# Kernel optimization log

Hardware: AMD Instinct MI355X
Metric: run time of the kernel (lower is better)

The kernel has to match this reference:

```python
import jax, jax.numpy as jnp
import numpy as np

N, DIN, DOUT = 8192, 256, 128
NEG_SLOPE = 0.01         # F.leaky_relu default
MASK_VAL = -9.0e15       # from the torch source


def setup_inputs() -> dict:
    key = jax.random.key(0)
    kx, kadj, kW, kbW, ka1, ka2, kba = jax.random.split(key, 7)
    x = jax.random.normal(kx, (N, DIN), dtype=jnp.float32)
    adj = jax.random.randint(kadj, (N, N), 0, 2, dtype=jnp.int32)
    # Linear W: input_dim -> output_dim
    W = jax.random.normal(kW, (DIN, DOUT), dtype=jnp.float32) * (1.0 / np.sqrt(DIN))
    bW = jax.random.normal(kbW, (DOUT,), dtype=jnp.float32) * 0.01
    # Linear a: 2*output_dim -> 1, split into the h_i part (a1) and h_j part (a2)
    a1 = jax.random.normal(ka1, (DOUT,), dtype=jnp.float32) * (1.0 / np.sqrt(2 * DOUT))
    a2 = jax.random.normal(ka2, (DOUT,), dtype=jnp.float32) * (1.0 / np.sqrt(2 * DOUT))
    ba = jax.random.normal(kba, (), dtype=jnp.float32) * 0.01
    return {"x": x, "adj": adj, "W": W, "bW": bW, "a1": a1, "a2": a2, "ba": ba}


def reference(x, adj, W, bW, a1, a2, ba):
    # h = W x + b  -> [N, DOUT]
    h = x @ W + bW
    # e[i,j] = leaky_relu(a . [h_i, h_j] + ba) = leaky_relu(a1.h_i + a2.h_j + ba)
    s_src = h @ a1            # [N]
    s_dst = h @ a2            # [N]
    e = s_src[:, None] + s_dst[None, :] + ba   # [N, N]
    e = jnp.where(e > 0, e, NEG_SLOPE * e)
    # mask non-edges, row softmax over neighbors j
    e = jnp.where(adj > 0, e, MASK_VAL)
    alpha = jax.nn.softmax(e, axis=1)          # [N, N]
    # dropout is identity in eval mode (dropout_rate=0)
    return alpha @ h                            # [N, DOUT]
```

## Files before the change

### kernel.cpp

```cpp
#include <hip/hip_runtime.h>
#include <hip/hip_bf16.h>


#define NN 8192
#define DIN 256
#define DOUT 128
#define LOG2E 1.4426950408889634f

typedef __attribute__((ext_vector_type(8))) short short8;
typedef __attribute__((ext_vector_type(4))) float floatx4;

__global__ void prep_wt(const float* __restrict__ W, __hip_bfloat16* __restrict__ WT) {
    int e = blockIdx.x * blockDim.x + threadIdx.x;
    if (e < DIN * DOUT) {
        int k = e >> 7;
        int d = e & 127;
        WT[d * DIN + k] = __float2bfloat16(W[e]);
    }
}

__global__ __launch_bounds__(256, 4) void gat_h(
    const float* __restrict__ x, const __hip_bfloat16* __restrict__ WT,
    const float* __restrict__ bW, const float* __restrict__ a1, const float* __restrict__ a2,
    __hip_bfloat16* __restrict__ hbB, float* __restrict__ s_src, float* __restrict__ s_dst) {
    int tid = threadIdx.x;
    int w = tid >> 6, lane = tid & 63;
    int lm = lane & 15, lq = lane >> 4;
    int i0 = blockIdx.x * 32;
    int r0 = (w >> 1) * 16;
    int c0 = (w & 1) * 64;

    __shared__ float s1s[32], s2s[32];
    if (tid < 32) { s1s[tid] = 0.f; s2s[tid] = 0.f; }
    __syncthreads();

    floatx4 acc[4] = {};
#pragma unroll
    for (int kk = 0; kk < DIN; kk += 32) {
        const float4* xp = (const float4*)&x[(size_t)(i0 + r0 + lm) * DIN + kk + lq * 8];
        float4 xa = xp[0], xb = xp[1];
        union { short8 v; __hip_bfloat16 h[8]; } af;
        af.h[0] = __float2bfloat16(xa.x); af.h[1] = __float2bfloat16(xa.y);
        af.h[2] = __float2bfloat16(xa.z); af.h[3] = __float2bfloat16(xa.w);
        af.h[4] = __float2bfloat16(xb.x); af.h[5] = __float2bfloat16(xb.y);
        af.h[6] = __float2bfloat16(xb.z); af.h[7] = __float2bfloat16(xb.w);
#pragma unroll
        for (int t = 0; t < 4; t++) {
            int d = c0 + 16 * t + lm;
            short8 bf = *(const short8*)&WT[(size_t)d * DIN + kk + lq * 8];
            acc[t] = __builtin_amdgcn_mfma_f32_16x16x32_bf16(af.v, bf, acc[t], 0, 0, 0);
        }
    }
    float s1[4] = {0.f, 0.f, 0.f, 0.f}, s2[4] = {0.f, 0.f, 0.f, 0.f};
#pragma unroll
    for (int t = 0; t < 4; t++) {
        int d = c0 + 16 * t + lm;
        int f = (c0 >> 4) + t;
        float A1 = a1[d], A2 = a2[d], B = bW[d];
#pragma unroll
        for (int r = 0; r < 4; r++) {
            int k = r0 + lq * 4 + r;
            float h = acc[t][r] + B;
            hbB[(size_t)blockIdx.x * 4096 + f * 512 + (k >> 3) * 128 + lm * 8 + (k & 7)] =
                __float2bfloat16(h);
            s1[r] += h * A1;
            s2[r] += h * A2;
        }
    }
#pragma unroll
    for (int r = 0; r < 4; r++) {
        for (int m = 1; m < 16; m <<= 1) {
            s1[r] += __shfl_xor(s1[r], m, 64);
            s2[r] += __shfl_xor(s2[r], m, 64);
        }
    }
    if (lm == 0) {
#pragma unroll
        for (int r = 0; r < 4; r++) {
            int row = r0 + lq * 4 + r;
            atomicAdd(&s1s[row], s1[r]);
            atomicAdd(&s2s[row], s2[r]);
        }
    }
    __syncthreads();
    if (tid < 32) {
        s_src[i0 + tid] = s1s[tid] * LOG2E;
        s_dst[i0 + tid] = s2s[tid] * LOG2E;
    }
}

template <int NJT>
__global__ void build_mask(const int* __restrict__ adj, unsigned char* __restrict__ mask) {
    size_t gid = (size_t)blockIdx.x * blockDim.x + threadIdx.x;
    const int4* a = (const int4*)(adj + gid * 8);
    int4 v0 = a[0], v1 = a[1];
    unsigned int b = 0;
    b |= (v0.x != 0) ? 1u : 0u;
    b |= (v0.y != 0) ? 2u : 0u;
    b |= (v0.z != 0) ? 4u : 0u;
    b |= (v0.w != 0) ? 8u : 0u;
    b |= (v1.x != 0) ? 16u : 0u;
    b |= (v1.y != 0) ? 32u : 0u;
    b |= (v1.z != 0) ? 64u : 0u;
    b |= (v1.w != 0) ? 128u : 0u;
    unsigned int g = (unsigned int)gid & (NJT * 4 - 1);
    size_t pos = (gid & ~(size_t)(NJT * 4 - 1)) | ((g & 3) * NJT + (g >> 2));
    mask[pos] = (unsigned char)b;
}

template <int NJT>
__global__ __launch_bounds__(256, 4) void gat_attn(
    const unsigned char* __restrict__ mask, const float* __restrict__ s_src,
    const float* __restrict__ s_dst, const float* __restrict__ ba_p,
    const __hip_bfloat16* __restrict__ hbB,
    float* __restrict__ num, float* __restrict__ lpart) {
    int tid = threadIdx.x;
    int w = tid >> 6, lane = tid & 63;
    int lm = lane & 15, lq = lane >> 4;
    int b = blockIdx.x;
    int ib = b & 127;
    int jh = b >> 7;
    int i0 = ib * 64 + w * 16;
    int jb0 = jh * (NJT * 32);

    const unsigned char* mrow = mask + (size_t)(i0 + lm) * (NN / 8) + jh * (NJT * 4) + lq * NJT;
    union { uint4 v[NJT / 16]; unsigned int u[NJT / 4]; } mr;
#pragma unroll
    for (int q = 0; q < NJT / 16; q++) mr.v[q] = ((const uint4*)mrow)[q];

    float ssi = s_src[i0 + lm] + ba_p[0] * LOG2E;
    const float* sd = s_dst + jb0 + lq * 8;
    const __hip_bfloat16* hb = hbB + ((size_t)(jh * NJT) * 8) * 512 + lane * 8;

    floatx4 acc[8] = {};
    floatx4 accd = {};
    const short8 ones = { 0x3F80, 0x3F80, 0x3F80, 0x3F80, 0x3F80, 0x3F80, 0x3F80, 0x3F80 };

#pragma unroll
    for (int t = 0; t < NJT; t++) {
        unsigned int cm = (mr.u[t >> 2] >> ((t & 3) * 8)) & 0xFFu;
        float4 cd0 = *(const float4*)(sd + t * 32);
        float4 cd1 = *(const float4*)(sd + t * 32 + 4);
        float p[8];
        {
            float e;
            e = ssi + cd0.x; e = fmaxf(e, 0.01f * e); p[0] = (cm & 1u)   ? __builtin_amdgcn_exp2f(e) : 0.f;
            e = ssi + cd0.y; e = fmaxf(e, 0.01f * e); p[1] = (cm & 2u)   ? __builtin_amdgcn_exp2f(e) : 0.f;
            e = ssi + cd0.z; e = fmaxf(e, 0.01f * e); p[2] = (cm & 4u)   ? __builtin_amdgcn_exp2f(e) : 0.f;
            e = ssi + cd0.w; e = fmaxf(e, 0.01f * e); p[3] = (cm & 8u)   ? __builtin_amdgcn_exp2f(e) : 0.f;
            e = ssi + cd1.x; e = fmaxf(e, 0.01f * e); p[4] = (cm & 16u)  ? __builtin_amdgcn_exp2f(e) : 0.f;
            e = ssi + cd1.y; e = fmaxf(e, 0.01f * e); p[5] = (cm & 32u)  ? __builtin_amdgcn_exp2f(e) : 0.f;
            e = ssi + cd1.z; e = fmaxf(e, 0.01f * e); p[6] = (cm & 64u)  ? __builtin_amdgcn_exp2f(e) : 0.f;
            e = ssi + cd1.w; e = fmaxf(e, 0.01f * e); p[7] = (cm & 128u) ? __builtin_amdgcn_exp2f(e) : 0.f;
        }
        union { short8 v; __hip_bfloat162 q[4]; } af;
        af.q[0] = __float22bfloat162_rn(make_float2(p[0], p[1]));
        af.q[1] = __float22bfloat162_rn(make_float2(p[2], p[3]));
        af.q[2] = __float22bfloat162_rn(make_float2(p[4], p[5]));
        af.q[3] = __float22bfloat162_rn(make_float2(p[6], p[7]));

        const __hip_bfloat16* hbt = hb + (size_t)t * 8 * 512;
#pragma unroll
        for (int f = 0; f < 8; f++) {
            short8 bf = *(const short8*)(hbt + f * 512);
            acc[f] = __builtin_amdgcn_mfma_f32_16x16x32_bf16(af.v, bf, acc[f], 0, 0, 0);
        }
        accd = __builtin_amdgcn_mfma_f32_16x16x32_bf16(af.v, ones, accd, 0, 0, 0);
    }

    float* nb = num + ((size_t)jh * NN + i0) * DOUT;
#pragma unroll
    for (int f = 0; f < 8; f++)
#pragma unroll
        for (int r = 0; r < 4; r++)
            nb[(size_t)(lq * 4 + r) * DOUT + f * 16 + lm] = acc[f][r];
    if (lm == 0) {
#pragma unroll
        for (int r = 0; r < 4; r++)
            lpart[(size_t)jh * NN + i0 + lq * 4 + r] = accd[r];
    }
}

__global__ void gat_combine(const float* __restrict__ num, const float* __restrict__ lpart,
                            float* __restrict__ out, int jsplit) {
    int gid = blockIdx.x * blockDim.x + threadIdx.x;
    int idx = gid * 4;
    int i = idx >> 7;
    float den = 0.f;
    for (int s = 0; s < jsplit; s++) den += lpart[(size_t)s * NN + i];
    float inv = 1.0f / den;
    float4 o = make_float4(0.f, 0.f, 0.f, 0.f);
    for (int s = 0; s < jsplit; s++) {
        float4 n = *(const float4*)&num[(size_t)s * NN * DOUT + idx];
        o.x += n.x; o.y += n.y; o.z += n.z; o.w += n.w;
    }
    o.x *= inv; o.y *= inv; o.z *= inv; o.w *= inv;
    *(float4*)&out[idx] = o;
}

extern "C" void kernel_launch(void* const* d_in, const int* in_sizes, int n_in,
                              void* d_out, int out_size, void* d_ws, size_t ws_size,
                              hipStream_t stream) {
    const float* x  = (const float*)d_in[0];
    const int* adj  = (const int*)d_in[1];
    const float* W  = (const float*)d_in[2];
    const float* bW = (const float*)d_in[3];
    const float* a1 = (const float*)d_in[4];
    const float* a2 = (const float*)d_in[5];
    const float* ba = (const float*)d_in[6];
    float* out = (float*)d_out;

    char* ws = (char*)d_ws;
    __hip_bfloat16* hbB  = (__hip_bfloat16*)ws;
    __hip_bfloat16* WT   = (__hip_bfloat16*)(ws + 2097152);
    float* s_src         = (float*)(ws + 2162688);
    float* s_dst         = (float*)(ws + 2195456);
    float* lpart         = (float*)(ws + 2228224);
    unsigned char* mask  = (unsigned char*)(ws + 2490368);
    float* num           = (float*)(ws + 10878976);

    int jsplit = (ws_size >= 10878976 + (size_t)8 * NN * DOUT * 4) ? 8 : 4;

    prep_wt<<<128, 256, 0, stream>>>(W, WT);
    gat_h<<<256, 256, 0, stream>>>(x, WT, bW, a1, a2, hbB, s_src, s_dst);
    if (jsplit == 8) {
        build_mask<32><<<32768, 256, 0, stream>>>(adj, mask);
        gat_attn<32><<<1024, 256, 0, stream>>>(mask, s_src, s_dst, ba, hbB, num, lpart);
    } else {
        build_mask<64><<<32768, 256, 0, stream>>>(adj, mask);
        gat_attn<64><<<512, 256, 0, stream>>>(mask, s_src, s_dst, ba, hbB, num, lpart);
    }
    gat_combine<<<1024, 256, 0, stream>>>(num, lpart, out, jsplit);
}
```

Measured before the change: 459.1 us.

## Compute two 16-row tiles per wave to reuse h fragments across MFMAs

Each wave now handles 32 query rows (two 16-row MFMA tiles) instead of 16. Every loaded bf16 h fragment feeds two MFMAs, which halves h load traffic per unit of work. The j dimension is split into 16 chunks instead of 8 so the grid stays at 1024 blocks, and launch bounds drop to 3 waves per SIMD to leave room for the doubled accumulator registers. The costs are larger partial-sum buffers for the combine kernel, more register pressure and lower occupancy.

```diff
diff --git a/kernel.cpp b/kernel.cpp
--- a/kernel.cpp
+++ b/kernel.cpp
@@ -108,8 +108,29 @@
     mask[pos] = (unsigned char)b;
 }
 
+__device__ inline short8 make_pfrag(unsigned int cm, float ssi, float4 cd0, float4 cd1,
+                                    floatx4* accd, const short8 ones) {
+    float p[8];
+    float e;
+    e = ssi + cd0.x; e = fmaxf(e, 0.01f * e); p[0] = (cm & 1u)   ? __builtin_amdgcn_exp2f(e) : 0.f;
+    e = ssi + cd0.y; e = fmaxf(e, 0.01f * e); p[1] = (cm & 2u)   ? __builtin_amdgcn_exp2f(e) : 0.f;
+    e = ssi + cd0.z; e = fmaxf(e, 0.01f * e); p[2] = (cm & 4u)   ? __builtin_amdgcn_exp2f(e) : 0.f;
+    e = ssi + cd0.w; e = fmaxf(e, 0.01f * e); p[3] = (cm & 8u)   ? __builtin_amdgcn_exp2f(e) : 0.f;
+    e = ssi + cd1.x; e = fmaxf(e, 0.01f * e); p[4] = (cm & 16u)  ? __builtin_amdgcn_exp2f(e) : 0.f;
+    e = ssi + cd1.y; e = fmaxf(e, 0.01f * e); p[5] = (cm & 32u)  ? __builtin_amdgcn_exp2f(e) : 0.f;
+    e = ssi + cd1.z; e = fmaxf(e, 0.01f * e); p[6] = (cm & 64u)  ? __builtin_amdgcn_exp2f(e) : 0.f;
+    e = ssi + cd1.w; e = fmaxf(e, 0.01f * e); p[7] = (cm & 128u) ? __builtin_amdgcn_exp2f(e) : 0.f;
+    union { short8 v; __hip_bfloat162 q[4]; } af;
+    af.q[0] = __float22bfloat162_rn(make_float2(p[0], p[1]));
+    af.q[1] = __float22bfloat162_rn(make_float2(p[2], p[3]));
+    af.q[2] = __float22bfloat162_rn(make_float2(p[4], p[5]));
+    af.q[3] = __float22bfloat162_rn(make_float2(p[6], p[7]));
+    *accd = __builtin_amdgcn_mfma_f32_16x16x32_bf16(af.v, ones, *accd, 0, 0, 0);
+    return af.v;
+}
+
 template <int NJT>
-__global__ __launch_bounds__(256, 4) void gat_attn(
+__global__ __launch_bounds__(256, 3) void gat_attn(
     const unsigned char* __restrict__ mask, const float* __restrict__ s_src,
     const float* __restrict__ s_dst, const float* __restrict__ ba_p,
     const __hip_bfloat16* __restrict__ hbB,
@@ -118,66 +139,63 @@
     int w = tid >> 6, lane = tid & 63;
     int lm = lane & 15, lq = lane >> 4;
     int b = blockIdx.x;
-    int ib = b & 127;
-    int jh = b >> 7;
-    int i0 = ib * 64 + w * 16;
+    int ib = b & 63;
+    int jh = b >> 6;
+    int i0 = ib * 128 + w * 32;
     int jb0 = jh * (NJT * 32);
 
-    const unsigned char* mrow = mask + (size_t)(i0 + lm) * (NN / 8) + jh * (NJT * 4) + lq * NJT;
-    union { uint4 v[NJT / 16]; unsigned int u[NJT / 4]; } mr;
-#pragma unroll
-    for (int q = 0; q < NJT / 16; q++) mr.v[q] = ((const uint4*)mrow)[q];
-
-    float ssi = s_src[i0 + lm] + ba_p[0] * LOG2E;
+    const unsigned char* mrow0 = mask + (size_t)(i0 + lm) * (NN / 8) + jh * (NJT * 4) + lq * NJT;
+    const unsigned char* mrow1 = mrow0 + (size_t)16 * (NN / 8);
+    union Mr { uint4 v[NJT / 16]; unsigned int u[NJT / 4]; };
+    Mr mr0, mr1;
+#pragma unroll
+    for (int q = 0; q < NJT / 16; q++) {
+        mr0.v[q] = ((const uint4*)mrow0)[q];
+        mr1.v[q] = ((const uint4*)mrow1)[q];
+    }
+
+    float ba = ba_p[0] * LOG2E;
+    float ssi0 = s_src[i0 + lm] + ba;
+    float ssi1 = s_src[i0 + 16 + lm] + ba;
     const float* sd = s_dst + jb0 + lq * 8;
     const __hip_bfloat16* hb = hbB + ((size_t)(jh * NJT) * 8) * 512 + lane * 8;
 
-    floatx4 acc[8] = {};
-    floatx4 accd = {};
+    floatx4 acc0[8] = {}, acc1[8] = {};
+    floatx4 accd0 = {}, accd1 = {};
     const short8 ones = { 0x3F80, 0x3F80, 0x3F80, 0x3F80, 0x3F80, 0x3F80, 0x3F80, 0x3F80 };
 
 #pragma unroll
     for (int t = 0; t < NJT; t++) {
-        unsigned int cm = (mr.u[t >> 2] >> ((t & 3) * 8)) & 0xFFu;
+        unsigned int cm0 = (mr0.u[t >> 2] >> ((t & 3) * 8)) & 0xFFu;
+        unsigned int cm1 = (mr1.u[t >> 2] >> ((t & 3) * 8)) & 0xFFu;
         float4 cd0 = *(const float4*)(sd + t * 32);
         float4 cd1 = *(const float4*)(sd + t * 32 + 4);
-        float p[8];
-        {
-            float e;
-            e = ssi + cd0.x; e = fmaxf(e, 0.01f * e); p[0] = (cm & 1u)   ? __builtin_amdgcn_exp2f(e) : 0.f;
-            e = ssi + cd0.y; e = fmaxf(e, 0.01f * e); p[1] = (cm & 2u)   ? __builtin_amdgcn_exp2f(e) : 0.f;
-            e = ssi + cd0.z; e = fmaxf(e, 0.01f * e); p[2] = (cm & 4u)   ? __builtin_amdgcn_exp2f(e) : 0.f;
-            e = ssi + cd0.w; e = fmaxf(e, 0.01f * e); p[3] = (cm & 8u)   ? __builtin_amdgcn_exp2f(e) : 0.f;
-            e = ssi + cd1.x; e = fmaxf(e, 0.01f * e); p[4] = (cm & 16u)  ? __builtin_amdgcn_exp2f(e) : 0.f;
-            e = ssi + cd1.y; e = fmaxf(e, 0.01f * e); p[5] = (cm & 32u)  ? __builtin_amdgcn_exp2f(e) : 0.f;
-            e = ssi + cd1.z; e = fmaxf(e, 0.01f * e); p[6] = (cm & 64u)  ? __builtin_amdgcn_exp2f(e) : 0.f;
-            e = ssi + cd1.w; e = fmaxf(e, 0.01f * e); p[7] = (cm & 128u) ? __builtin_amdgcn_exp2f(e) : 0.f;
-        }
-        union { short8 v; __hip_bfloat162 q[4]; } af;
-        af.q[0] = __float22bfloat162_rn(make_float2(p[0], p[1]));
-        af.q[1] = __float22bfloat162_rn(make_float2(p[2], p[3]));
-        af.q[2] = __float22bfloat162_rn(make_float2(p[4], p[5]));
-        af.q[3] = __float22bfloat162_rn(make_float2(p[6], p[7]));
+        short8 af0 = make_pfrag(cm0, ssi0, cd0, cd1, &accd0, ones);
+        short8 af1 = make_pfrag(cm1, ssi1, cd0, cd1, &accd1, ones);
 
         const __hip_bfloat16* hbt = hb + (size_t)t * 8 * 512;
 #pragma unroll
         for (int f = 0; f < 8; f++) {
             short8 bf = *(const short8*)(hbt + f * 512);
-            acc[f] = __builtin_amdgcn_mfma_f32_16x16x32_bf16(af.v, bf, acc[f], 0, 0, 0);
-        }
-        accd = __builtin_amdgcn_mfma_f32_16x16x32_bf16(af.v, ones, accd, 0, 0, 0);
+            acc0[f] = __builtin_amdgcn_mfma_f32_16x16x32_bf16(af0, bf, acc0[f], 0, 0, 0);
+            acc1[f] = __builtin_amdgcn_mfma_f32_16x16x32_bf16(af1, bf, acc1[f], 0, 0, 0);
+        }
     }
 
     float* nb = num + ((size_t)jh * NN + i0) * DOUT;
 #pragma unroll
     for (int f = 0; f < 8; f++)
 #pragma unroll
-        for (int r = 0; r < 4; r++)
-            nb[(size_t)(lq * 4 + r) * DOUT + f * 16 + lm] = acc[f][r];
+        for (int r = 0; r < 4; r++) {
+            nb[(size_t)(lq * 4 + r) * DOUT + f * 16 + lm] = acc0[f][r];
+            nb[(size_t)(16 + lq * 4 + r) * DOUT + f * 16 + lm] = acc1[f][r];
+        }
     if (lm == 0) {
 #pragma unroll
-        for (int r = 0; r < 4; r++)
-            lpart[(size_t)jh * NN + i0 + lq * 4 + r] = accd[r];
+        for (int r = 0; r < 4; r++) {
+            lpart[(size_t)jh * NN + i0 + lq * 4 + r] = accd0[r];
+            lpart[(size_t)jh * NN + i0 + 16 + lq * 4 + r] = accd1[r];
+        }
     }
 }
 
@@ -216,19 +234,18 @@
     float* s_src         = (float*)(ws + 2162688);
     float* s_dst         = (float*)(ws + 2195456);
     float* lpart         = (float*)(ws + 2228224);
-    unsigned char* mask  = (unsigned char*)(ws + 2490368);
-    float* num           = (float*)(ws + 10878976);
-
-    int jsplit = (ws_size >= 10878976 + (size_t)8 * NN * DOUT * 4) ? 8 : 4;
-
+    unsigned char* mask  = (unsigned char*)(ws + 2752512);
+    float* num           = (float*)(ws + 11141120);
+
+    int jsplit = (ws_size >= 11141120 + (size_t)16 * NN * DOUT * 4) ? 16 : 8;
+
+    if (jsplit == 16) build_mask<16><<<32768, 256, 0, stream>>>(adj, mask);
+    else              build_mask<32><<<32768, 256, 0, stream>>>(adj, mask);
     prep_wt<<<128, 256, 0, stream>>>(W, WT);
     gat_h<<<256, 256, 0, stream>>>(x, WT, bW, a1, a2, hbB, s_src, s_dst);
-    if (jsplit == 8) {
-        build_mask<32><<<32768, 256, 0, stream>>>(adj, mask);
-        gat_attn<32><<<1024, 256, 0, stream>>>(mask, s_src, s_dst, ba, hbB, num, lpart);
-    } else {
-        build_mask<64><<<32768, 256, 0, stream>>>(adj, mask);
-        gat_attn<64><<<512, 256, 0, stream>>>(mask, s_src, s_dst, ba, hbB, num, lpart);
-    }
+    if (jsplit == 16)
+        gat_attn<16><<<1024, 256, 0, stream>>>(mask, s_src, s_dst, ba, hbB, num, lpart);
+    else
+        gat_attn<32><<<512, 256, 0, stream>>>(mask, s_src, s_dst, ba, hbB, num, lpart);
     gat_combine<<<1024, 256, 0, stream>>>(num, lpart, out, jsplit);
 }
```

New measurement: 437.3 us. -4.8%, faster.
